# Kernel tuning notes

Hardware: AMD Instinct MI355X
Metric: run time of the kernel (lower is better)

## Reference

```python
import jax, jax.numpy as jnp
import numpy as np

N_NODES = 100000
N_EDGES = 3200000
IN_DIM = 256
EMB_DIM = 64
BATCH = 4096
WEIGHT_DECAY = 1e-4


def setup_inputs() -> dict:
    key = jax.random.key(0)
    ks = jax.random.split(key, 8)
    feats = jax.random.normal(ks[0], (N_NODES, IN_DIM), dtype=jnp.float32)
    W = jax.random.normal(ks[1], (IN_DIM, EMB_DIM), dtype=jnp.float32) * (1.0 / np.sqrt(IN_DIM))
    edge_row = jax.random.randint(ks[2], (N_EDGES,), 0, N_NODES, dtype=jnp.int32)
    edge_col = jax.random.randint(ks[3], (N_EDGES,), 0, N_NODES, dtype=jnp.int32)
    edge_val = jax.random.uniform(ks[4], (N_EDGES,), dtype=jnp.float32) * 0.05  # normalized adj weights
    idx1 = jax.random.randint(ks[5], (BATCH,), 0, N_NODES, dtype=jnp.int32)
    idx2 = jax.random.randint(ks[6], (BATCH,), 0, N_NODES, dtype=jnp.int32)
    neg_idx = jax.random.randint(ks[7], (BATCH,), 0, N_NODES, dtype=jnp.int32)
    return {"feats": feats, "W": W, "edge_row": edge_row, "edge_col": edge_col,
            "edge_val": edge_val, "idx1": idx1, "idx2": idx2, "neg_idx": neg_idx}


def reference(feats, W, edge_row, edge_col, edge_val, idx1, idx2, neg_idx):
    # GraphConvolution: tanh( A_sparse @ (X @ W) ), A in COO form
    xw = feats @ W                                              # [N, D]
    msgs = edge_val[:, None] * xw[edge_col]                     # [E, D] gather + scale
    h = jax.ops.segment_sum(msgs, edge_row, num_segments=N_NODES)  # sparse-dense matmul
    h = jnp.tanh(h)
    # tf.nn.l2_normalize(embedding, 1)
    sq = jnp.sum(h * h, axis=1, keepdims=True)
    emb = h * jax.lax.rsqrt(jnp.maximum(sq, 1e-12))             # [N, D]
    # embedding lookups
    o1, o2, on = emb[idx1], emb[idx2], emb[neg_idx]             # [B, D] each
    y_ui = jnp.sum(o1 * o2, axis=1)
    y_uj = jnp.sum(o1 * on, axis=1)
    # BPR loss + weight decay (tf.nn.l2_loss = 0.5*sum(x^2))
    bpr = jnp.sum(-jax.nn.log_sigmoid(y_ui - y_uj))
    loss = (bpr + WEIGHT_DECAY * 0.5 * jnp.sum(emb * emb)) / jnp.float32(BATCH)
    return loss
```

## Files before the change

### kernel.cpp

```cpp
#include <hip/hip_runtime.h>
#include <cmath>

#define N_NODES 100000
#define N_EDGES 3200000
#define IN_DIM 256
#define EMB 64
#define BATCH 4096
#define MWAVES 6250
#define NBUCK 782
#define BROWS 128
#define BSTRIDE 4608
#define EPB 4096

typedef unsigned long long u64;
typedef unsigned int u32;
typedef unsigned short u16;
typedef __attribute__((ext_vector_type(8))) short bf16x8;
typedef __attribute__((ext_vector_type(4))) float f32x4;

__device__ __forceinline__ float wave_sum(float v) {
#pragma unroll
    for (int m = 1; m < 64; m <<= 1) v += __shfl_xor(v, m, 64);
    return v;
}

__device__ __forceinline__ u16 f2bf_rne(float f) {
    u32 u = __float_as_uint(f);
    u32 r = ((u >> 16) & 1u) + 0x7FFFu;
    return (u16)((u + r) >> 16);
}

__device__ __forceinline__ float bf2f(u32 bits16) {
    return __uint_as_float(bits16 << 16);
}

__global__ __launch_bounds__(256) void mfma_gemm_kernel(const float* __restrict__ feats,
                                                        const float* __restrict__ W,
                                                        u16* __restrict__ xwb) {
    __shared__ u16 wlds[32 * 64 * 8];
    const int tid = threadIdx.x;
    for (int idx = tid; idx < 32 * 64; idx += 256) {
        const int f = idx >> 6, lane = idx & 63;
        const int kt = f >> 2, nt = f & 3;
        const int k0 = kt * 32 + (lane >> 4) * 8;
        const int n  = nt * 16 + (lane & 15);
        u32 buf[4];
#pragma unroll
        for (int jj = 0; jj < 4; ++jj) {
            u16 lo = f2bf_rne(W[(size_t)(k0 + 2 * jj) * EMB + n]);
            u16 hi = f2bf_rne(W[(size_t)(k0 + 2 * jj + 1) * EMB + n]);
            buf[jj] = (u32)lo | ((u32)hi << 16);
        }
        *(uint4*)&wlds[idx * 8] = *(uint4*)buf;
    }
    __syncthreads();

    const int wave = tid >> 6, lane = tid & 63;
    const int wid = blockIdx.x * 4 + wave;
    if (wid >= MWAVES) return;
    const int row0 = wid * 16;
    const int arow = row0 + (lane & 15);
    const int kbase = (lane >> 4) * 8;
    const float* fr = feats + (size_t)arow * IN_DIM + kbase;

    float4 av[16];
#pragma unroll
    for (int kt = 0; kt < 8; ++kt) {
        av[2 * kt]     = *(const float4*)(fr + kt * 32);
        av[2 * kt + 1] = *(const float4*)(fr + kt * 32 + 4);
    }

    f32x4 acc[4] = {};
    const u16* wl = &wlds[lane * 8];
#pragma unroll
    for (int kt = 0; kt < 8; ++kt) {
        float4 a0 = av[2 * kt], a1 = av[2 * kt + 1];
        u32 ab[4];
        ab[0] = (u32)f2bf_rne(a0.x) | ((u32)f2bf_rne(a0.y) << 16);
        ab[1] = (u32)f2bf_rne(a0.z) | ((u32)f2bf_rne(a0.w) << 16);
        ab[2] = (u32)f2bf_rne(a1.x) | ((u32)f2bf_rne(a1.y) << 16);
        ab[3] = (u32)f2bf_rne(a1.z) | ((u32)f2bf_rne(a1.w) << 16);
        bf16x8 afrag = *(bf16x8*)ab;
#pragma unroll
        for (int nt = 0; nt < 4; ++nt) {
            bf16x8 bfrag = *(const bf16x8*)&wl[(kt * 4 + nt) * 512];
            acc[nt] = __builtin_amdgcn_mfma_f32_16x16x32_bf16(afrag, bfrag, acc[nt], 0, 0, 0);
        }
    }
    const int rb = row0 + (lane >> 4) * 4;
    const int cb = lane & 15;
#pragma unroll
    for (int nt = 0; nt < 4; ++nt)
#pragma unroll
        for (int r = 0; r < 4; ++r)
            xwb[(size_t)(rb + r) * EMB + nt * 16 + cb] = f2bf_rne(acc[nt][r]);
}

__global__ __launch_bounds__(256) void passA_kernel(const int* __restrict__ erow,
                                                    const int* __restrict__ ecol,
                                                    const float* __restrict__ eval,
                                                    u32* __restrict__ gcursor,
                                                    u64* __restrict__ sorted) {
    __shared__ u64 stage[EPB];
    __shared__ u32 hist[1024];
    __shared__ u32 offs[1024];
    __shared__ u32 cursor[1024];
    __shared__ u32 gbase[1024];
    __shared__ u32 partial[256];

    const int tid = threadIdx.x;
    const int e0 = blockIdx.x * EPB;
    const int total = min(EPB, N_EDGES - e0);

    for (int i = tid; i < 1024; i += 256) hist[i] = 0;
    __syncthreads();

    u64 ent[16];
    int eb[16];
#pragma unroll
    for (int j = 0; j < 16; ++j) {
        const int e = e0 + j * 256 + tid;
        if (e < N_EDGES) {
            const int r = erow[e];
            const int c = ecol[e];
            const u16 vb = f2bf_rne(eval[e]);
            ent[j] = (u64)(u32)r | ((u64)(u32)c << 17) | ((u64)vb << 34);
            eb[j] = r >> 7;
            atomicAdd(&hist[eb[j]], 1u);
        } else {
            eb[j] = -1;
        }
    }
    __syncthreads();

    u32 local[4], s = 0;
#pragma unroll
    for (int q = 0; q < 4; ++q) {
        local[q] = s;
        s += hist[4 * tid + q];
    }
    partial[tid] = s;
    __syncthreads();
    for (int off = 1; off < 256; off <<= 1) {
        u32 x = (tid >= off) ? partial[tid - off] : 0;
        __syncthreads();
        partial[tid] += x;
        __syncthreads();
    }
    const u32 base = partial[tid] - s;
#pragma unroll
    for (int q = 0; q < 4; ++q) {
        offs[4 * tid + q] = base + local[q];
        cursor[4 * tid + q] = base + local[q];
    }
    __syncthreads();

#pragma unroll
    for (int j = 0; j < 16; ++j) {
        if (eb[j] >= 0) {
            u32 pos = atomicAdd(&cursor[eb[j]], 1u);
            stage[pos] = ent[j];
        }
    }
    __syncthreads();

    for (int b = tid; b < 1024; b += 256) {
        const u32 cnt = cursor[b] - offs[b];
        gbase[b] = cnt ? atomicAdd(&gcursor[b], cnt) : 0;
    }
    __syncthreads();

    for (int i = tid; i < total; i += 256) {
        const u64 p = stage[i];
        const int b = (int)(p & 0x1FFFFu) >> 7;
        const u32 gpos = gbase[b] + ((u32)i - offs[b]);
        if (gpos < BSTRIDE) sorted[(size_t)b * BSTRIDE + gpos] = p;
    }
}

__global__ __launch_bounds__(1024, 8) void gather_kernel(const u16* __restrict__ xwb,
                                                         u64* __restrict__ sorted,
                                                         const u32* __restrict__ gcursor,
                                                         float* __restrict__ accumA) {
    __shared__ u64 stage[BSTRIDE];
    __shared__ u32 rhist[BROWS], roff[BROWS], rcur[BROWS], sc[BROWS];
    __shared__ float part[16];
    const int tid = threadIdx.x, wave = tid >> 6, lane = tid & 63;
    const int b = blockIdx.x;
    u64* gbase = sorted + (size_t)b * BSTRIDE;
    const int cnt = min((int)gcursor[b], BSTRIDE);

    if (tid < BROWS) rhist[tid] = 0;
    __syncthreads();

    u64 ent[5];
    int nloc = 0;
    for (int i = tid; i < cnt; i += 1024) {
        u64 p = gbase[i];
        ent[nloc++] = p;
        atomicAdd(&rhist[(int)(p & 127u)], 1u);
    }
    __syncthreads();

    if (tid < BROWS) sc[tid] = rhist[tid];
    __syncthreads();
    for (int off = 1; off < BROWS; off <<= 1) {
        u32 x = (tid < BROWS && tid >= off) ? sc[tid - off] : 0;
        __syncthreads();
        if (tid < BROWS) sc[tid] += x;
        __syncthreads();
    }
    if (tid < BROWS) {
        roff[tid] = sc[tid] - rhist[tid];
        rcur[tid] = sc[tid] - rhist[tid];
    }
    __syncthreads();

    for (int j = 0; j < nloc; ++j) {
        const u64 p = ent[j];
        const u32 pos = atomicAdd(&rcur[(int)(p & 127u)], 1u);
        stage[pos] = p;
    }
    __syncthreads();

    u16* embp = (u16*)gbase;
    float wd = 0.f;
    for (int rr = 0; rr < 8; ++rr) {
        const int r = wave * 8 + rr;
        const int s0 = roff[r], n = rhist[r];
        float acc = 0.f;
        int j = s0;
        const int e2 = s0 + n;
        for (; j + 7 < e2; j += 8) {
            u64 p0 = stage[j],     p1 = stage[j + 1], p2 = stage[j + 2], p3 = stage[j + 3];
            u64 p4 = stage[j + 4], p5 = stage[j + 5], p6 = stage[j + 6], p7 = stage[j + 7];
            float x0 = bf2f(xwb[(size_t)((p0 >> 17) & 0x1FFFFu) * EMB + lane]);
            float x1 = bf2f(xwb[(size_t)((p1 >> 17) & 0x1FFFFu) * EMB + lane]);
            float x2 = bf2f(xwb[(size_t)((p2 >> 17) & 0x1FFFFu) * EMB + lane]);
            float x3 = bf2f(xwb[(size_t)((p3 >> 17) & 0x1FFFFu) * EMB + lane]);
            float x4 = bf2f(xwb[(size_t)((p4 >> 17) & 0x1FFFFu) * EMB + lane]);
            float x5 = bf2f(xwb[(size_t)((p5 >> 17) & 0x1FFFFu) * EMB + lane]);
            float x6 = bf2f(xwb[(size_t)((p6 >> 17) & 0x1FFFFu) * EMB + lane]);
            float x7 = bf2f(xwb[(size_t)((p7 >> 17) & 0x1FFFFu) * EMB + lane]);
            acc += bf2f((u32)(p0 >> 34) & 0xFFFFu) * x0 + bf2f((u32)(p1 >> 34) & 0xFFFFu) * x1;
            acc += bf2f((u32)(p2 >> 34) & 0xFFFFu) * x2 + bf2f((u32)(p3 >> 34) & 0xFFFFu) * x3;
            acc += bf2f((u32)(p4 >> 34) & 0xFFFFu) * x4 + bf2f((u32)(p5 >> 34) & 0xFFFFu) * x5;
            acc += bf2f((u32)(p6 >> 34) & 0xFFFFu) * x6 + bf2f((u32)(p7 >> 34) & 0xFFFFu) * x7;
        }
        for (; j < e2; ++j) {
            u64 p = stage[j];
            acc += bf2f((u32)(p >> 34) & 0xFFFFu) * bf2f(xwb[(size_t)((p >> 17) & 0x1FFFFu) * EMB + lane]);
        }
        float x = tanhf(acc);
        float sq = wave_sum(x * x);
        if (b * BROWS + r < N_NODES)
            embp[r * EMB + lane] = f2bf_rne(x * rsqrtf(fmaxf(sq, 1e-12f)));
        wd += sq / fmaxf(sq, 1e-12f);
    }
    if (lane == 0) part[wave] = wd;
    __syncthreads();
    if (tid == 0) {
        float v = 0.f;
#pragma unroll
        for (int w = 0; w < 16; ++w) v += part[w];
        unsafeAtomicAdd(&accumA[b & 255], v);
    }
}

__device__ __forceinline__ float emb_ld(const u64* __restrict__ sorted, int row, int lane) {
    const u16* rp = (const u16*)(sorted + (size_t)(row >> 7) * BSTRIDE) + (row & 127) * EMB;
    return bf2f(rp[lane]);
}

__global__ __launch_bounds__(256) void bpr_kernel(const u64* __restrict__ sorted,
                                                  const int* __restrict__ idx1,
                                                  const int* __restrict__ idx2,
                                                  const int* __restrict__ nidx,
                                                  float* __restrict__ accumB) {
    const int wave = threadIdx.x >> 6, lane = threadIdx.x & 63;
    const int i = blockIdx.x * 4 + wave;
    float o1 = emb_ld(sorted, idx1[i], lane);
    float o2 = emb_ld(sorted, idx2[i], lane);
    float on = emb_ld(sorted, nidx[i], lane);
    float yui = wave_sum(o1 * o2);
    float yuj = wave_sum(o1 * on);
    if (lane == 0) {
        float x = yui - yuj;
        float li = (x > 0.f) ? log1pf(expf(-x)) : (-x + log1pf(expf(x)));
        unsafeAtomicAdd(&accumB[i & 255], li);
    }
}

__global__ __launch_bounds__(64) void finalize_kernel(const float* __restrict__ accumA,
                                                      const float* __restrict__ accumB,
                                                      float* __restrict__ out) {
    const int t = threadIdx.x;
    float wd = 0.f, bp = 0.f;
#pragma unroll
    for (int k = 0; k < 4; ++k) {
        wd += accumA[t + 64 * k];
        bp += accumB[t + 64 * k];
    }
    wd = wave_sum(wd);
    bp = wave_sum(bp);
    if (t == 0) out[0] = (bp + 1e-4f * 0.5f * wd) / (float)BATCH;
}

extern "C" void kernel_launch(void* const* d_in, const int* in_sizes, int n_in,
                              void* d_out, int out_size, void* d_ws, size_t ws_size,
                              hipStream_t stream) {
    const float* feats = (const float*)d_in[0];
    const float* W     = (const float*)d_in[1];
    const int*   erow  = (const int*)d_in[2];
    const int*   ecol  = (const int*)d_in[3];
    const float* eval  = (const float*)d_in[4];
    const int*   idx1  = (const int*)d_in[5];
    const int*   idx2  = (const int*)d_in[6];
    const int*   nidx  = (const int*)d_in[7];
    float* out = (float*)d_out;

    u16*   xwb     = (u16*)d_ws;
    u64*   sorted  = (u64*)(xwb + (size_t)N_NODES * EMB);
    u32*   gcursor = (u32*)(sorted + (size_t)NBUCK * BSTRIDE);
    float* accumA  = (float*)(gcursor + 1024);
    float* accumB  = accumA + 256;

    hipMemsetAsync(gcursor, 0, (1024 + 512) * sizeof(u32), stream);

    mfma_gemm_kernel<<<(MWAVES + 3) / 4, 256, 0, stream>>>(feats, W, xwb);
    passA_kernel<<<(N_EDGES + EPB - 1) / EPB, 256, 0, stream>>>(erow, ecol, eval, gcursor, sorted);
    gather_kernel<<<NBUCK, 1024, 0, stream>>>(xwb, sorted, gcursor, accumA);
    bpr_kernel<<<BATCH / 4, 256, 0, stream>>>(sorted, idx1, idx2, nidx, accumB);
    finalize_kernel<<<1, 64, 0, stream>>>(accumA, accumB, out);
}
```

Before: 344.3 us.

## Gather two bf16 columns per lane with half-wave edge split and padded segments

Rewrites the gather kernel's inner loop so each lane loads a 32-bit pair of bf16 columns. The two half-waves process alternating edges and their partial sums are combined with a shuffle. Each row's edge segment is padded to a multiple of 8 with zero entries, and entries are pre-decoded into a byte offset plus an fp32 weight, so the loop has no remainder handling and little unpacking. The block shrinks to 512 threads with 16 rows per wave. The goal is fewer, wider global loads per edge and less ALU work, at the cost of extra shared memory for padding and fewer threads per block.

After: 345.9 us. No clear change (+0.5%).

```diff
diff --git a/kernel.cpp b/kernel.cpp
--- a/kernel.cpp
+++ b/kernel.cpp
@@ -10,6 +10,7 @@
 #define NBUCK 782
 #define BROWS 128
 #define BSTRIDE 4608
+#define PSTRIDE 5504
 #define EPB 4096
 
 typedef unsigned long long u64;
@@ -178,13 +179,13 @@
     }
 }
 
-__global__ __launch_bounds__(1024, 8) void gather_kernel(const u16* __restrict__ xwb,
-                                                         u64* __restrict__ sorted,
-                                                         const u32* __restrict__ gcursor,
-                                                         float* __restrict__ accumA) {
-    __shared__ u64 stage[BSTRIDE];
+__global__ __launch_bounds__(512, 6) void gather_kernel(const u16* __restrict__ xwb,
+                                                        u64* __restrict__ sorted,
+                                                        const u32* __restrict__ gcursor,
+                                                        float* __restrict__ accumA) {
+    __shared__ u64 stage[PSTRIDE];
     __shared__ u32 rhist[BROWS], roff[BROWS], rcur[BROWS], sc[BROWS];
-    __shared__ float part[16];
+    __shared__ float part[8];
     const int tid = threadIdx.x, wave = tid >> 6, lane = tid & 63;
     const int b = blockIdx.x;
     u64* gbase = sorted + (size_t)b * BSTRIDE;
@@ -193,16 +194,16 @@
     if (tid < BROWS) rhist[tid] = 0;
     __syncthreads();
 
-    u64 ent[5];
+    u64 ent[9];
     int nloc = 0;
-    for (int i = tid; i < cnt; i += 1024) {
+    for (int i = tid; i < cnt; i += 512) {
         u64 p = gbase[i];
         ent[nloc++] = p;
         atomicAdd(&rhist[(int)(p & 127u)], 1u);
     }
     __syncthreads();
 
-    if (tid < BROWS) sc[tid] = rhist[tid];
+    if (tid < BROWS) sc[tid] = (rhist[tid] + 7u) & ~7u;
     __syncthreads();
     for (int off = 1; off < BROWS; off <<= 1) {
         u32 x = (tid < BROWS && tid >= off) ? sc[tid - off] : 0;
@@ -211,50 +212,69 @@
         __syncthreads();
     }
     if (tid < BROWS) {
-        roff[tid] = sc[tid] - rhist[tid];
-        rcur[tid] = sc[tid] - rhist[tid];
+        const u32 r0 = sc[tid] - ((rhist[tid] + 7u) & ~7u);
+        roff[tid] = r0;
+        rcur[tid] = r0;
     }
     __syncthreads();
 
     for (int j = 0; j < nloc; ++j) {
         const u64 p = ent[j];
         const u32 pos = atomicAdd(&rcur[(int)(p & 127u)], 1u);
-        stage[pos] = p;
+        const u32 coff = (((u32)(p >> 17)) & 0x1FFFFu) << 7;
+        const u32 v32  = (((u32)(p >> 34)) & 0xFFFFu) << 16;
+        stage[pos] = (u64)coff | ((u64)v32 << 32);
+    }
+    __syncthreads();
+
+    if (tid < BROWS) {
+        const int e = roff[tid] + rhist[tid];
+        const int pe = roff[tid] + (int)((rhist[tid] + 7u) & ~7u);
+        for (int k = e; k < pe; ++k) stage[k] = 0ull;
     }
     __syncthreads();
 
     u16* embp = (u16*)gbase;
+    const int lhalf = lane >> 5;
+    const int loff = (lane & 31) * 4;
+    const char* xwc = (const char*)xwb;
     float wd = 0.f;
-    for (int rr = 0; rr < 8; ++rr) {
-        const int r = wave * 8 + rr;
-        const int s0 = roff[r], n = rhist[r];
-        float acc = 0.f;
-        int j = s0;
-        const int e2 = s0 + n;
-        for (; j + 7 < e2; j += 8) {
-            u64 p0 = stage[j],     p1 = stage[j + 1], p2 = stage[j + 2], p3 = stage[j + 3];
-            u64 p4 = stage[j + 4], p5 = stage[j + 5], p6 = stage[j + 6], p7 = stage[j + 7];
-            float x0 = bf2f(xwb[(size_t)((p0 >> 17) & 0x1FFFFu) * EMB + lane]);
-            float x1 = bf2f(xwb[(size_t)((p1 >> 17) & 0x1FFFFu) * EMB + lane]);
-            float x2 = bf2f(xwb[(size_t)((p2 >> 17) & 0x1FFFFu) * EMB + lane]);
-            float x3 = bf2f(xwb[(size_t)((p3 >> 17) & 0x1FFFFu) * EMB + lane]);
-            float x4 = bf2f(xwb[(size_t)((p4 >> 17) & 0x1FFFFu) * EMB + lane]);
-            float x5 = bf2f(xwb[(size_t)((p5 >> 17) & 0x1FFFFu) * EMB + lane]);
-            float x6 = bf2f(xwb[(size_t)((p6 >> 17) & 0x1FFFFu) * EMB + lane]);
-            float x7 = bf2f(xwb[(size_t)((p7 >> 17) & 0x1FFFFu) * EMB + lane]);
-            acc += bf2f((u32)(p0 >> 34) & 0xFFFFu) * x0 + bf2f((u32)(p1 >> 34) & 0xFFFFu) * x1;
-            acc += bf2f((u32)(p2 >> 34) & 0xFFFFu) * x2 + bf2f((u32)(p3 >> 34) & 0xFFFFu) * x3;
-            acc += bf2f((u32)(p4 >> 34) & 0xFFFFu) * x4 + bf2f((u32)(p5 >> 34) & 0xFFFFu) * x5;
-            acc += bf2f((u32)(p6 >> 34) & 0xFFFFu) * x6 + bf2f((u32)(p7 >> 34) & 0xFFFFu) * x7;
-        }
-        for (; j < e2; ++j) {
-            u64 p = stage[j];
-            acc += bf2f((u32)(p >> 34) & 0xFFFFu) * bf2f(xwb[(size_t)((p >> 17) & 0x1FFFFu) * EMB + lane]);
-        }
-        float x = tanhf(acc);
-        float sq = wave_sum(x * x);
-        if (b * BROWS + r < N_NODES)
-            embp[r * EMB + lane] = f2bf_rne(x * rsqrtf(fmaxf(sq, 1e-12f)));
+    for (int rr = 0; rr < 16; ++rr) {
+        const int r = wave * 16 + rr;
+        const int n8 = (int)((rhist[r] + 7u) & ~7u);
+        float acc0 = 0.f, acc1 = 0.f;
+        const u64* sp = &stage[roff[r] + lhalf];
+        for (int j = 0; j < n8; j += 8, sp += 8) {
+            u64 cv0 = sp[0], cv1 = sp[2], cv2 = sp[4], cv3 = sp[6];
+            u32 x0 = *(const u32*)(xwc + ((u32)cv0 + loff));
+            u32 x1 = *(const u32*)(xwc + ((u32)cv1 + loff));
+            u32 x2 = *(const u32*)(xwc + ((u32)cv2 + loff));
+            u32 x3 = *(const u32*)(xwc + ((u32)cv3 + loff));
+            float v0 = __uint_as_float((u32)(cv0 >> 32));
+            float v1 = __uint_as_float((u32)(cv1 >> 32));
+            float v2 = __uint_as_float((u32)(cv2 >> 32));
+            float v3 = __uint_as_float((u32)(cv3 >> 32));
+            acc0 += v0 * __uint_as_float(x0 << 16);
+            acc1 += v0 * __uint_as_float(x0 & 0xFFFF0000u);
+            acc0 += v1 * __uint_as_float(x1 << 16);
+            acc1 += v1 * __uint_as_float(x1 & 0xFFFF0000u);
+            acc0 += v2 * __uint_as_float(x2 << 16);
+            acc1 += v2 * __uint_as_float(x2 & 0xFFFF0000u);
+            acc0 += v3 * __uint_as_float(x3 << 16);
+            acc1 += v3 * __uint_as_float(x3 & 0xFFFF0000u);
+        }
+        acc0 += __shfl_xor(acc0, 32, 64);
+        acc1 += __shfl_xor(acc1, 32, 64);
+        const float t0 = tanhf(acc0);
+        const float t1 = tanhf(acc1);
+        float sq = t0 * t0 + t1 * t1;
+#pragma unroll
+        for (int m = 1; m < 32; m <<= 1) sq += __shfl_xor(sq, m, 64);
+        const float rn = rsqrtf(fmaxf(sq, 1e-12f));
+        if (lhalf == 0 && b * BROWS + r < N_NODES) {
+            const u32 o = (u32)f2bf_rne(t0 * rn) | ((u32)f2bf_rne(t1 * rn) << 16);
+            *(u32*)&embp[r * EMB + (lane & 31) * 2] = o;
+        }
         wd += sq / fmaxf(sq, 1e-12f);
     }
     if (lane == 0) part[wave] = wd;
@@ -262,7 +282,7 @@
     if (tid == 0) {
         float v = 0.f;
 #pragma unroll
-        for (int w = 0; w < 16; ++w) v += part[w];
+        for (int w = 0; w < 8; ++w) v += part[w];
         unsafeAtomicAdd(&accumA[b & 255], v);
     }
 }
@@ -329,7 +349,7 @@
 
     mfma_gemm_kernel<<<(MWAVES + 3) / 4, 256, 0, stream>>>(feats, W, xwb);
     passA_kernel<<<(N_EDGES + EPB - 1) / EPB, 256, 0, stream>>>(erow, ecol, eval, gcursor, sorted);
-    gather_kernel<<<NBUCK, 1024, 0, stream>>>(xwb, sorted, gcursor, accumA);
+    gather_kernel<<<NBUCK, 512, 0, stream>>>(xwb, sorted, gcursor, accumA);
     bpr_kernel<<<BATCH / 4, 256, 0, stream>>>(sorted, idx1, idx2, nidx, accumB);
     finalize_kernel<<<1, 64, 0, stream>>>(accumA, accumB, out);
 }
```
